# Performance work log

Measured on AMD Instinct MI355X. Metric: run time of the kernel, lower is better.

The kernel has to match this reference:

```python
import jax, jax.numpy as jnp
import numpy as np

P = 10                      # half-window; kernel size K = 2P+1 = 21
GROUPS = ((0, 1000), (1000, 2000))  # hardcoded self.group = [0, 1000, 2000]


def setup_inputs() -> dict:
    key = jax.random.key(0)
    k1, k2, k3 = jax.random.split(key, 3)
    n, T, D = 16, 1024, 2000
    x = jax.random.normal(k1, (n, T, D), dtype=jnp.float32)
    W0 = jax.random.normal(k2, (D, 2 * P + 1), dtype=jnp.float32)
    W1 = jax.random.normal(k3, (D, 2 * P + 1), dtype=jnp.float32)
    return {"x": x, "W0": W0, "W1": W1}


def _shift_attention(x, Ws):
    n, T, D = x.shape
    K = 2 * P + 1
    # x_padded built from the ORIGINAL x under no_grad (detached)
    xp = jax.lax.stop_gradient(jnp.pad(x, ((0, 0), (P, P), (0, 0))))
    cur = x
    for Wi, (s, e) in zip(Ws, GROUPS):
        # dynamic per-timestep window weights: (n, T, K)
        w = jnp.einsum('ntd,dk->ntk', cur, Wi)
        xg = xp[:, :, s:e]  # (n, T+2P, g)
        # out[:, t, :] = sum_k w[:, t, k] * xg[:, t+k, :]  (windowed combine)
        out = w[:, :, 0, None] * xg[:, 0:T, :]
        for k in range(1, K):  # fixed small tap count, not a data-dim loop
            out = out + w[:, :, k, None] * xg[:, k:k + T, :]
        # in-place column update -> group 1 sees group 0's result in 'cur'
        cur = cur.at[:, :, s:e].set(out)
    return cur


def reference(x, W0, W1):
    return _shift_attention(x, (W0, W1))
```

## Files before the change

kernel.cpp:

```cpp
#include <hip/hip_runtime.h>

#define N_  16
#define T_  1024
#define D_  2000
#define K_  21
#define P_  10
#define NT_ (N_*T_)

__global__ void k_padW(const float* __restrict__ W0, const float* __restrict__ W1,
                       float* __restrict__ W0p, float* __restrict__ W1p) {
    int gid = blockIdx.x * blockDim.x + threadIdx.x;
    if (gid >= D_ * 24) return;
    int d = gid / 24, kk = gid - d * 24;
    W0p[gid] = (kk < K_) ? W0[d * K_ + kk] : 0.f;
    W1p[gid] = (kk < K_) ? W1[d * K_ + kk] : 0.f;
}

__global__ __launch_bounds__(256)
void k_coef(const float* __restrict__ x,
            const float* __restrict__ W0p, const float* __restrict__ W1p,
            float* __restrict__ q0, float* __restrict__ q1,
            float* __restrict__ q2, float* __restrict__ q3,
            float* __restrict__ m0, float* __restrict__ m1,
            float* __restrict__ p1, float* __restrict__ p2,
            float* __restrict__ p3) {
    __shared__ float lds[5888];
    const int tid  = threadIdx.x;
    const int lane = tid & 63;
    const int w    = __builtin_amdgcn_readfirstlane(tid >> 6);
    const int rg   = blockIdx.x >> 2;
    const int h    = blockIdx.x & 3;
    const int r0   = rg * 64;
    const int d0q  = h * 512;

    float a0[K_], am[K_], ap[K_];
#pragma unroll
    for (int k = 0; k < K_; ++k) { a0[k] = 0.f; am[k] = 0.f; ap[k] = 0.f; }

    const int srow = tid >> 2;
    const int sc4  = (tid & 3) * 2;
    float4 ra, rb;

    auto load_tile = [&](int dt) {
        const int d = d0q + dt + sc4 * 4;
        const float* p = x + (size_t)(r0 + srow) * D_ + d;
        ra = (d     < D_) ? *reinterpret_cast<const float4*>(p)
                          : make_float4(0.f, 0.f, 0.f, 0.f);
        rb = (d + 4 < D_) ? *reinterpret_cast<const float4*>(p + 4)
                          : make_float4(0.f, 0.f, 0.f, 0.f);
    };
    auto write_tile = [&](int buf) {
        float* b = lds + buf * 2112 + srow * 33 + sc4 * 4;
        b[0] = ra.x; b[1] = ra.y; b[2] = ra.z; b[3] = ra.w;
        b[4] = rb.x; b[5] = rb.y; b[6] = rb.z; b[7] = rb.w;
    };

    load_tile(0);
    write_tile(0);
    __syncthreads();

    for (int t = 0; t < 16; ++t) {
        if (t < 15) load_tile((t + 1) * 32);
        const float* xrow = lds + (t & 1) * 2112 + lane * 33;
#pragma unroll
        for (int c = 0; c < 8; ++c) {
            const int col = w * 8 + c;
            const int d = d0q + t * 32 + col;
            const int du = (d < D_) ? d : (D_ - 1);
            const float xv = xrow[col];
            const float* __restrict__ wr0 = W0p + du * 24;
            const float* __restrict__ wr1 = W1p + du * 24;
#pragma unroll
            for (int k = 0; k < K_; ++k) a0[k] = fmaf(xv, wr0[k], a0[k]);
            if (d < 1000) {
#pragma unroll
                for (int k = 0; k < K_; ++k) am[k] = fmaf(xv, wr1[k], am[k]);
            } else {
#pragma unroll
                for (int k = 0; k < K_; ++k) ap[k] = fmaf(xv, wr1[k], ap[k]);
            }
        }
        if (t < 15) write_tile((t + 1) & 1);
        __syncthreads();
    }

    auto reduce_store = [&](const float* acc, float* dst) {
        __syncthreads();
#pragma unroll
        for (int k = 0; k < K_; ++k) lds[tid * 23 + k] = acc[k];
        __syncthreads();
        for (int o = tid; o < 64 * K_; o += 256) {
            int t = o / K_, j = o - t * K_;
            float s = lds[t * 23 + j] + lds[(64 + t) * 23 + j] +
                      lds[(128 + t) * 23 + j] + lds[(192 + t) * 23 + j];
            dst[(size_t)(r0 + t) * K_ + j] = s;
        }
    };

    float* const qd[4] = {q0, q1, q2, q3};
    reduce_store(a0, qd[h]);
    if (h == 0) reduce_store(am, m0);
    if (h == 1) { reduce_store(am, m1); reduce_store(ap, p1); }
    if (h == 2) reduce_store(ap, p2);
    if (h == 3) reduce_store(ap, p3);
}

__global__ __launch_bounds__(256)
void k_finish(const float* __restrict__ q0, const float* __restrict__ q1,
              const float* __restrict__ q2, const float* __restrict__ q3,
              const float* __restrict__ m0, const float* __restrict__ m1,
              const float* __restrict__ p1, const float* __restrict__ p2,
              const float* __restrict__ p3,
              float* __restrict__ w0f, float* __restrict__ w1f) {
    __shared__ float w0s[64 * K_];
    __shared__ float Ms[84 * K_];
    const int tid = threadIdx.x;
    const int r0 = blockIdx.x * 64;

    for (int o = tid; o < 64 * K_; o += 256) {
        size_t g = (size_t)r0 * K_ + o;
        w0s[o] = q0[g] + q1[g] + q2[g] + q3[g];
    }
    for (int o = tid; o < 84 * K_; o += 256) {
        int i = o / K_, j = o - i * K_;
        int rr = r0 - P_ + i;
        float v = 0.f;
        if (rr >= 0 && rr < NT_) {
            size_t g = (size_t)rr * K_ + j;
            v = m0[g] + m1[g];
        }
        Ms[o] = v;
    }
    __syncthreads();

    for (int o = tid; o < 64 * K_; o += 256) {
        int row = o / K_, k = o - row * K_;
        size_t g = (size_t)(r0 + row) * K_ + k;
        float acc = p1[g] + p2[g] + p3[g];
        int t = (r0 + row) & (T_ - 1);
#pragma unroll
        for (int j = 0; j < K_; ++j) {
            int tt = t + j - P_;
            if (tt >= 0 && tt < T_)
                acc = fmaf(w0s[row * K_ + j], Ms[(row + j) * K_ + k], acc);
        }
        w1f[g] = acc;
        w0f[g] = w0s[o];
    }
}

__global__ __launch_bounds__(256)
void k_conv(const float* __restrict__ x, const float* __restrict__ w0,
            const float* __restrict__ w1, float* __restrict__ out) {
    __shared__ float xsl[84][128];
    __shared__ float wc[64 * K_];
    const int b = blockIdx.x;
    const int grp = b >> 11;
    const float* __restrict__ coef = grp ? w1 : w0;
    const int dbase = grp * 1000;
    const int bb = b & 2047;
    const int dseg = bb & 7;
    const int tch = (bb >> 3) & 15;
    const int nn = bb >> 7;
    const int t0 = tch * 64;
    const int tid = threadIdx.x;
    const float* xb = x + (size_t)nn * T_ * D_;

    {
        const int scol = tid & 31, srow0 = tid >> 5;
#pragma unroll
        for (int pass = 0; pass < 11; ++pass) {
            int rr = srow0 + pass * 8;
            if (rr < 84) {
                int u = t0 - P_ + rr;
                int dl = dseg * 128 + scol * 4;
                float4 v = make_float4(0.f, 0.f, 0.f, 0.f);
                if (u >= 0 && u < T_ && dl < 1000)
                    v = *reinterpret_cast<const float4*>(xb + (size_t)u * D_ + dbase + dl);
                *reinterpret_cast<float4*>(&xsl[rr][scol * 4]) = v;
            }
        }
    }
    for (int o = tid; o < 64 * K_; o += 256) {
        int tl = o / K_, k = o - tl * K_;
        wc[o] = coef[((size_t)nn * T_ + t0 + tl) * K_ + k];
    }
    __syncthreads();

    const int col = tid & 31;
    const int tsub = tid >> 5;
    const int tl0 = tsub * 8;
    float4 acc[8];
#pragma unroll
    for (int g = 0; g < 8; ++g) acc[g] = make_float4(0.f, 0.f, 0.f, 0.f);

#pragma unroll
    for (int ul = 0; ul < 28; ++ul) {
        const int rr = tl0 + ul;
        const float4 xf = *reinterpret_cast<const float4*>(&xsl[rr][col * 4]);
#pragma unroll
        for (int g = 0; g < 8; ++g) {
            const int k = ul - g;
            if (k >= 0 && k < K_) {
                const float c = wc[(tl0 + g) * K_ + k];
                acc[g].x = fmaf(c, xf.x, acc[g].x);
                acc[g].y = fmaf(c, xf.y, acc[g].y);
                acc[g].z = fmaf(c, xf.z, acc[g].z);
                acc[g].w = fmaf(c, xf.w, acc[g].w);
            }
        }
    }

    const int dl = dseg * 128 + col * 4;
    if (dl < 1000) {
#pragma unroll
        for (int g = 0; g < 8; ++g) {
            float* dst = out + ((size_t)nn * T_ + t0 + tl0 + g) * D_ + dbase + dl;
            *reinterpret_cast<float4*>(dst) = acc[g];
        }
    }
}

extern "C" void kernel_launch(void* const* d_in, const int* in_sizes, int n_in,
                              void* d_out, int out_size, void* d_ws, size_t ws_size,
                              hipStream_t stream) {
    const float* x  = (const float*)d_in[0];
    const float* W0 = (const float*)d_in[1];
    const float* W1 = (const float*)d_in[2];
    float* out = (float*)d_out;
    float* ws  = (float*)d_ws;

    const size_t CW = 344064;
    float* W0p = ws;
    float* W1p = ws + 48000;
    float* q0  = ws + 96000 + 0 * CW;
    float* q1  = ws + 96000 + 1 * CW;
    float* q2  = ws + 96000 + 2 * CW;
    float* q3  = ws + 96000 + 3 * CW;
    float* m0  = ws + 96000 + 4 * CW;
    float* m1  = ws + 96000 + 5 * CW;
    float* p1  = ws + 96000 + 6 * CW;
    float* p2  = ws + 96000 + 7 * CW;
    float* p3  = ws + 96000 + 8 * CW;
    float* w0f = ws + 96000 + 9 * CW;
    float* w1f = ws + 96000 + 10 * CW;

    hipLaunchKernelGGL(k_padW, dim3(188), dim3(256), 0, stream, W0, W1, W0p, W1p);
    hipLaunchKernelGGL(k_coef, dim3(1024), dim3(256), 0, stream,
                       x, W0p, W1p, q0, q1, q2, q3, m0, m1, p1, p2, p3);
    hipLaunchKernelGGL(k_finish, dim3(256), dim3(256), 0, stream,
                       q0, q1, q2, q3, m0, m1, p1, p2, p3, w0f, w1f);
    hipLaunchKernelGGL(k_conv, dim3(4096), dim3(256), 0, stream, x, w0f, w1f, out);
}
```

Measured before the change: 468.6 us.

## Split coef reduction into aligned 500-column quarters and use sliding-window conv

k_coef now splits the D dimension into four 500-column quarters so each block holds only two accumulator sets instead of three. This removes the divergent group branch and one reduce/store pass. The clamped index becomes a uniform scalar moved to a VGPR, and weight rows are loaded as float4 with a launch-bounds occupancy hint. k_conv is restructured so each thread keeps a rolling 21-row register window of float2 x values and computes 16 consecutive outputs, with coefficients padded to 24-wide rows for vector LDS loads; the trade is more registers and half-width columns per thread.

```diff
diff --git a/kernel.cpp b/kernel.cpp
--- a/kernel.cpp
+++ b/kernel.cpp
@@ -16,14 +16,13 @@
     W1p[gid] = (kk < K_) ? W1[d * K_ + kk] : 0.f;
 }
 
-__global__ __launch_bounds__(256)
+__global__ __launch_bounds__(256, 3)
 void k_coef(const float* __restrict__ x,
             const float* __restrict__ W0p, const float* __restrict__ W1p,
             float* __restrict__ q0, float* __restrict__ q1,
             float* __restrict__ q2, float* __restrict__ q3,
-            float* __restrict__ m0, float* __restrict__ m1,
-            float* __restrict__ p1, float* __restrict__ p2,
-            float* __restrict__ p3) {
+            float* __restrict__ mp0, float* __restrict__ mp1,
+            float* __restrict__ mp2, float* __restrict__ mp3) {
     __shared__ float lds[5888];
     const int tid  = threadIdx.x;
     const int lane = tid & 63;
@@ -31,26 +30,26 @@
     const int rg   = blockIdx.x >> 2;
     const int h    = blockIdx.x & 3;
     const int r0   = rg * 64;
-    const int d0q  = h * 512;
-
-    float a0[K_], am[K_], ap[K_];
-#pragma unroll
-    for (int k = 0; k < K_; ++k) { a0[k] = 0.f; am[k] = 0.f; ap[k] = 0.f; }
+    const int d0q  = h * 500;
+
+    float a0[K_], a1[K_];
+#pragma unroll
+    for (int k = 0; k < K_; ++k) { a0[k] = 0.f; a1[k] = 0.f; }
 
     const int srow = tid >> 2;
-    const int sc4  = (tid & 3) * 2;
+    const int sf4  = (tid & 3) * 2;
     float4 ra, rb;
 
     auto load_tile = [&](int dt) {
-        const int d = d0q + dt + sc4 * 4;
-        const float* p = x + (size_t)(r0 + srow) * D_ + d;
-        ra = (d     < D_) ? *reinterpret_cast<const float4*>(p)
-                          : make_float4(0.f, 0.f, 0.f, 0.f);
-        rb = (d + 4 < D_) ? *reinterpret_cast<const float4*>(p + 4)
-                          : make_float4(0.f, 0.f, 0.f, 0.f);
+        const int c0 = dt + sf4 * 4;
+        const float* p = x + (size_t)(r0 + srow) * D_ + d0q + c0;
+        ra = (c0 < 500)     ? *reinterpret_cast<const float4*>(p)
+                            : make_float4(0.f, 0.f, 0.f, 0.f);
+        rb = (c0 + 4 < 500) ? *reinterpret_cast<const float4*>(p + 4)
+                            : make_float4(0.f, 0.f, 0.f, 0.f);
     };
     auto write_tile = [&](int buf) {
-        float* b = lds + buf * 2112 + srow * 33 + sc4 * 4;
+        float* b = lds + buf * 2112 + srow * 33 + sf4 * 4;
         b[0] = ra.x; b[1] = ra.y; b[2] = ra.z; b[3] = ra.w;
         b[4] = rb.x; b[5] = rb.y; b[6] = rb.z; b[7] = rb.w;
     };
@@ -61,23 +60,32 @@
 
     for (int t = 0; t < 16; ++t) {
         if (t < 15) load_tile((t + 1) * 32);
+        const int cw = (t < 15) ? 32 : 20;
         const float* xrow = lds + (t & 1) * 2112 + lane * 33;
 #pragma unroll
         for (int c = 0; c < 8; ++c) {
             const int col = w * 8 + c;
-            const int d = d0q + t * 32 + col;
-            const int du = (d < D_) ? d : (D_ - 1);
-            const float xv = xrow[col];
-            const float* __restrict__ wr0 = W0p + du * 24;
-            const float* __restrict__ wr1 = W1p + du * 24;
-#pragma unroll
-            for (int k = 0; k < K_; ++k) a0[k] = fmaf(xv, wr0[k], a0[k]);
-            if (d < 1000) {
-#pragma unroll
-                for (int k = 0; k < K_; ++k) am[k] = fmaf(xv, wr1[k], am[k]);
-            } else {
-#pragma unroll
-                for (int k = 0; k < K_; ++k) ap[k] = fmaf(xv, wr1[k], ap[k]);
+            if (col < cw) {
+                const int d = d0q + t * 32 + col;
+                int duv;
+                asm("v_mov_b32 %0, %1" : "=v"(duv) : "s"(d));
+                const float* w0r = W0p + duv * 24;
+                const float* w1r = W1p + duv * 24;
+                float wa[21], wb[21];
+#pragma unroll
+                for (int j = 0; j < 5; ++j) {
+                    *reinterpret_cast<float4*>(&wa[4 * j]) =
+                        *reinterpret_cast<const float4*>(w0r + 4 * j);
+                    *reinterpret_cast<float4*>(&wb[4 * j]) =
+                        *reinterpret_cast<const float4*>(w1r + 4 * j);
+                }
+                wa[20] = w0r[20];
+                wb[20] = w1r[20];
+                const float xv = xrow[col];
+#pragma unroll
+                for (int k = 0; k < K_; ++k) a0[k] = fmaf(xv, wa[k], a0[k]);
+#pragma unroll
+                for (int k = 0; k < K_; ++k) a1[k] = fmaf(xv, wb[k], a1[k]);
             }
         }
         if (t < 15) write_tile((t + 1) & 1);
@@ -90,27 +98,24 @@
         for (int k = 0; k < K_; ++k) lds[tid * 23 + k] = acc[k];
         __syncthreads();
         for (int o = tid; o < 64 * K_; o += 256) {
-            int t = o / K_, j = o - t * K_;
-            float s = lds[t * 23 + j] + lds[(64 + t) * 23 + j] +
-                      lds[(128 + t) * 23 + j] + lds[(192 + t) * 23 + j];
-            dst[(size_t)(r0 + t) * K_ + j] = s;
+            int tt = o / K_, j = o - tt * K_;
+            float s = lds[tt * 23 + j] + lds[(64 + tt) * 23 + j] +
+                      lds[(128 + tt) * 23 + j] + lds[(192 + tt) * 23 + j];
+            dst[(size_t)(r0 + tt) * K_ + j] = s;
         }
     };
 
     float* const qd[4] = {q0, q1, q2, q3};
+    float* const md[4] = {mp0, mp1, mp2, mp3};
     reduce_store(a0, qd[h]);
-    if (h == 0) reduce_store(am, m0);
-    if (h == 1) { reduce_store(am, m1); reduce_store(ap, p1); }
-    if (h == 2) reduce_store(ap, p2);
-    if (h == 3) reduce_store(ap, p3);
+    reduce_store(a1, md[h]);
 }
 
 __global__ __launch_bounds__(256)
 void k_finish(const float* __restrict__ q0, const float* __restrict__ q1,
               const float* __restrict__ q2, const float* __restrict__ q3,
-              const float* __restrict__ m0, const float* __restrict__ m1,
-              const float* __restrict__ p1, const float* __restrict__ p2,
-              const float* __restrict__ p3,
+              const float* __restrict__ mp0, const float* __restrict__ mp1,
+              const float* __restrict__ mp2, const float* __restrict__ mp3,
               float* __restrict__ w0f, float* __restrict__ w1f) {
     __shared__ float w0s[64 * K_];
     __shared__ float Ms[84 * K_];
@@ -127,7 +132,7 @@
         float v = 0.f;
         if (rr >= 0 && rr < NT_) {
             size_t g = (size_t)rr * K_ + j;
-            v = m0[g] + m1[g];
+            v = mp0[g] + mp1[g];
         }
         Ms[o] = v;
     }
@@ -136,7 +141,7 @@
     for (int o = tid; o < 64 * K_; o += 256) {
         int row = o / K_, k = o - row * K_;
         size_t g = (size_t)(r0 + row) * K_ + k;
-        float acc = p1[g] + p2[g] + p3[g];
+        float acc = mp2[g] + mp3[g];
         int t = (r0 + row) & (T_ - 1);
 #pragma unroll
         for (int j = 0; j < K_; ++j) {
@@ -150,18 +155,17 @@
 }
 
 __global__ __launch_bounds__(256)
-void k_conv(const float* __restrict__ x, const float* __restrict__ w0,
-            const float* __restrict__ w1, float* __restrict__ out) {
+void k_conv(const float* __restrict__ x, const float* __restrict__ w0f,
+            const float* __restrict__ w1f, float* __restrict__ out) {
     __shared__ float xsl[84][128];
-    __shared__ float wc[64 * K_];
+    __shared__ float wc[64 * 24];
     const int b = blockIdx.x;
-    const int grp = b >> 11;
-    const float* __restrict__ coef = grp ? w1 : w0;
+    const int dseg = b & 7;
+    const int tch  = (b >> 3) & 15;
+    const int nn   = (b >> 7) & 15;
+    const int grp  = b >> 11;
+    const float* __restrict__ coef = grp ? w1f : w0f;
     const int dbase = grp * 1000;
-    const int bb = b & 2047;
-    const int dseg = bb & 7;
-    const int tch = (bb >> 3) & 15;
-    const int nn = bb >> 7;
     const int t0 = tch * 64;
     const int tid = threadIdx.x;
     const float* xb = x + (size_t)nn * T_ * D_;
@@ -181,43 +185,42 @@
             }
         }
     }
-    for (int o = tid; o < 64 * K_; o += 256) {
-        int tl = o / K_, k = o - tl * K_;
-        wc[o] = coef[((size_t)nn * T_ + t0 + tl) * K_ + k];
+    for (int o = tid; o < 64 * 24; o += 256) {
+        int tl = o / 24, k = o - tl * 24;
+        wc[o] = (k < K_) ? coef[((size_t)nn * T_ + t0 + tl) * K_ + k] : 0.f;
     }
     __syncthreads();
 
-    const int col = tid & 31;
-    const int tsub = tid >> 5;
-    const int tl0 = tsub * 8;
-    float4 acc[8];
-#pragma unroll
-    for (int g = 0; g < 8; ++g) acc[g] = make_float4(0.f, 0.f, 0.f, 0.f);
-
-#pragma unroll
-    for (int ul = 0; ul < 28; ++ul) {
-        const int rr = tl0 + ul;
-        const float4 xf = *reinterpret_cast<const float4*>(&xsl[rr][col * 4]);
-#pragma unroll
-        for (int g = 0; g < 8; ++g) {
-            const int k = ul - g;
-            if (k >= 0 && k < K_) {
-                const float c = wc[(tl0 + g) * K_ + k];
-                acc[g].x = fmaf(c, xf.x, acc[g].x);
-                acc[g].y = fmaf(c, xf.y, acc[g].y);
-                acc[g].z = fmaf(c, xf.z, acc[g].z);
-                acc[g].w = fmaf(c, xf.w, acc[g].w);
-            }
-        }
-    }
-
-    const int dl = dseg * 128 + col * 4;
-    if (dl < 1000) {
-#pragma unroll
-        for (int g = 0; g < 8; ++g) {
-            float* dst = out + ((size_t)nn * T_ + t0 + tl0 + g) * D_ + dbase + dl;
-            *reinterpret_cast<float4*>(dst) = acc[g];
-        }
+    const int wv = tid >> 6, lane = tid & 63;
+    const int rw = wv * 16;
+    const int dcol = dseg * 128 + lane * 2;
+    const bool act = (dcol < 1000);
+
+    float2 win[21];
+#pragma unroll
+    for (int s = 0; s < 21; ++s)
+        win[s] = *reinterpret_cast<const float2*>(&xsl[rw + s][lane * 2]);
+
+    float* obase = out + ((size_t)nn * T_ + t0 + rw) * D_ + dbase + dcol;
+
+#pragma unroll
+    for (int i = 0; i < 16; ++i) {
+        float cfa[24];
+        const float4* cf = reinterpret_cast<const float4*>(&wc[(rw + i) * 24]);
+#pragma unroll
+        for (int j = 0; j < 5; ++j)
+            *reinterpret_cast<float4*>(&cfa[4 * j]) = cf[j];
+        cfa[20] = wc[(rw + i) * 24 + 20];
+        float2 acc = make_float2(0.f, 0.f);
+#pragma unroll
+        for (int k = 0; k < K_; ++k) {
+            const float2 xv = win[(i + k) % 21];
+            acc.x = fmaf(cfa[k], xv.x, acc.x);
+            acc.y = fmaf(cfa[k], xv.y, acc.y);
+        }
+        if (act) *reinterpret_cast<float2*>(obase + (size_t)i * D_) = acc;
+        if (i < 15)
+            win[i % 21] = *reinterpret_cast<const float2*>(&xsl[rw + i + 21][lane * 2]);
     }
 }
 
@@ -237,18 +240,17 @@
     float* q1  = ws + 96000 + 1 * CW;
     float* q2  = ws + 96000 + 2 * CW;
     float* q3  = ws + 96000 + 3 * CW;
-    float* m0  = ws + 96000 + 4 * CW;
-    float* m1  = ws + 96000 + 5 * CW;
-    float* p1  = ws + 96000 + 6 * CW;
-    float* p2  = ws + 96000 + 7 * CW;
-    float* p3  = ws + 96000 + 8 * CW;
-    float* w0f = ws + 96000 + 9 * CW;
-    float* w1f = ws + 96000 + 10 * CW;
+    float* mp0 = ws + 96000 + 4 * CW;
+    float* mp1 = ws + 96000 + 5 * CW;
+    float* mp2 = ws + 96000 + 6 * CW;
+    float* mp3 = ws + 96000 + 7 * CW;
+    float* w0f = ws + 96000 + 8 * CW;
+    float* w1f = ws + 96000 + 9 * CW;
 
     hipLaunchKernelGGL(k_padW, dim3(188), dim3(256), 0, stream, W0, W1, W0p, W1p);
     hipLaunchKernelGGL(k_coef, dim3(1024), dim3(256), 0, stream,
-                       x, W0p, W1p, q0, q1, q2, q3, m0, m1, p1, p2, p3);
+                       x, W0p, W1p, q0, q1, q2, q3, mp0, mp1, mp2, mp3);
     hipLaunchKernelGGL(k_finish, dim3(256), dim3(256), 0, stream,
-                       q0, q1, q2, q3, m0, m1, p1, p2, p3, w0f, w1f);
+                       q0, q1, q2, q3, mp0, mp1, mp2, mp3, w0f, w1f);
     hipLaunchKernelGGL(k_conv, dim3(4096), dim3(256), 0, stream, x, w0f, w1f, out);
 }
```

Result: faster. 438.5 us (-6.4%).
